# Performance work log

Measured on AMD Instinct MI355X. Metric: run time of the kernel, lower is better.

## Reference

```python
import jax, jax.numpy as jnp
import numpy as np
from jax import lax

EPS = 1e-5
DN = ('NCDHW', 'OIDHW', 'NCDHW')


def _instance_norm(x, w, b):
    # normalize over spatial dims per (batch, channel); biased variance like torch
    mu = jnp.mean(x, axis=(2, 3, 4), keepdims=True)
    var = jnp.mean((x - mu) ** 2, axis=(2, 3, 4), keepdims=True)
    xn = (x - mu) * lax.rsqrt(var + EPS)
    return xn * w[None, :, None, None, None] + b[None, :, None, None, None]


def _conv1x1(x, w, b):
    # w: [Cout, Cin]
    y = jnp.einsum('bcdhw,oc->bodhw', x, w)
    return y + b[None, :, None, None, None]


def _dwconv3(x, w, b):
    # depthwise 3x3x3, padding 1; w: [C, 1, 3, 3, 3]
    y = lax.conv_general_dilated(x, w, (1, 1, 1), 'SAME',
                                 dimension_numbers=DN,
                                 feature_group_count=w.shape[0])
    return y + b[None, :, None, None, None]


def setup_inputs() -> dict:
    key = jax.random.key(0)
    ks = jax.random.split(key, 8)
    C, half = 64, 32
    B, D, H, W = 1, 96, 96, 96
    s1 = 1.0 / np.sqrt(C)          # fan_in of 1x1 conv
    s3 = 1.0 / np.sqrt(27.0)       # fan_in of depthwise 3x3x3
    return {
        'x': jax.random.normal(ks[0], (B, C, D, H, W), jnp.float32),
        'norm_w': jnp.ones((C,), jnp.float32),
        'norm_b': jnp.zeros((C,), jnp.float32),
        'in_proj_w': jax.random.normal(ks[1], (C, C), jnp.float32) * s1,
        'in_proj_b': jnp.zeros((C,), jnp.float32),
        'conv_ssm_w': jax.random.normal(ks[2], (half, 1, 3, 3, 3), jnp.float32) * s3,
        'conv_ssm_b': jnp.zeros((half,), jnp.float32),
        'mamba_w': jax.random.normal(ks[3], (half, 1, 3, 3, 3), jnp.float32) * s3,
        'mamba_b': jnp.zeros((half,), jnp.float32),
        'conv_sym_w': jax.random.normal(ks[4], (half, 1, 3, 3, 3), jnp.float32) * s3,
        'conv_sym_b': jnp.zeros((half,), jnp.float32),
        'out_proj_w': jax.random.normal(ks[5], (C, C), jnp.float32) * s1,
        'out_proj_b': jnp.zeros((C,), jnp.float32),
    }


def reference(x, norm_w, norm_b, in_proj_w, in_proj_b,
              conv_ssm_w, conv_ssm_b, mamba_w, mamba_b,
              conv_sym_w, conv_sym_b, out_proj_w, out_proj_b):
    residual = x
    xp = _conv1x1(_instance_norm(x, norm_w, norm_b), in_proj_w, in_proj_b)
    half = xp.shape[1] // 2
    x1, x2 = xp[:, :half], xp[:, half:]
    # SSM branch (TriDirectionalMamba fallback = depthwise conv3)
    x1 = _dwconv3(jax.nn.silu(_dwconv3(x1, conv_ssm_w, conv_ssm_b)), mamba_w, mamba_b)
    # symmetric conv branch
    x2 = jax.nn.silu(_dwconv3(x2, conv_sym_w, conv_sym_b))
    y = _conv1x1(jnp.concatenate([x1, x2], axis=1), out_proj_w, out_proj_b)
    return y + residual
```

## Files before the change

### kernel.cpp

```cpp
#include <hip/hip_runtime.h>

typedef unsigned short u16;
typedef unsigned int u32;
typedef short bf16x8 __attribute__((ext_vector_type(8)));
typedef float f32x16 __attribute__((ext_vector_type(16)));
typedef u16 u16x8 __attribute__((ext_vector_type(8)));

#define DIM 96
#define PLANE (DIM*DIM)
#define S 884736
#define C 64
#define HALF 32
#define PARTS 16
#define EPS 1e-5f
#define DSPLIT 4
#define DCHUNK (DIM/DSPLIT)

#define RPAD 104
#define LROWS 18
#define LBUF (8 + LROWS*RPAD)

#define MFMA32(a,b,c) __builtin_amdgcn_mfma_f32_32x32x16_bf16(a,b,c,0,0,0)

__device__ __forceinline__ u16 f2bf(float f) {
  u32 u = __builtin_bit_cast(u32, f);
  return (u16)((u + 0x7FFFu + ((u >> 16) & 1u)) >> 16);
}
__device__ __forceinline__ float bf2f(u16 h) {
  return __builtin_bit_cast(float, (u32)h << 16);
}
__device__ __forceinline__ u32 cvt_pk_bf16(float lo, float hi) {
  u32 r;
  asm("v_cvt_pk_bf16_f32 %0, %1, %2" : "=v"(r) : "v"(lo), "v"(hi));
  return r;
}
__device__ __forceinline__ float silu(float v) { return v / (1.f + __expf(-v)); }
__device__ __forceinline__ u16x8 zero8() {
  u16x8 z;
  #pragma unroll
  for (int i = 0; i < 8; ++i) z[i] = 0;
  return z;
}

__global__ __launch_bounds__(256) void k1_stats(const float* __restrict__ x,
                                                u16* __restrict__ xb,
                                                float* __restrict__ psum,
                                                float* __restrict__ psq) {
  const int bid = blockIdx.x;
  const int ch = bid / PARTS, part = bid % PARTS;
  const int chunk = S / PARTS;
  const size_t base = (size_t)ch * S + (size_t)part * chunk;
  const float4* p = (const float4*)(x + base);
  ushort4* xb4 = (ushort4*)(xb + base);
  const int n4 = chunk / 4;
  float s = 0.f, q = 0.f;
  for (int i = threadIdx.x; i < n4; i += 256) {
    float4 v = p[i];
    s += (v.x + v.y) + (v.z + v.w);
    q += (v.x * v.x + v.y * v.y) + (v.z * v.z + v.w * v.w);
    union { u32 u[2]; ushort4 v4; } o;
    o.u[0] = cvt_pk_bf16(v.x, v.y);
    o.u[1] = cvt_pk_bf16(v.z, v.w);
    xb4[i] = o.v4;
  }
  #pragma unroll
  for (int off = 32; off > 0; off >>= 1) {
    s += __shfl_down(s, off);
    q += __shfl_down(q, off);
  }
  __shared__ float ls[4], lq[4];
  const int wid = threadIdx.x >> 6, lane = threadIdx.x & 63;
  if (lane == 0) { ls[wid] = s; lq[wid] = q; }
  __syncthreads();
  if (threadIdx.x == 0) {
    psum[bid] = (ls[0] + ls[1]) + (ls[2] + ls[3]);
    psq[bid]  = (lq[0] + lq[1]) + (lq[2] + lq[3]);
  }
}

__global__ __launch_bounds__(64) void k1b_prep(const float* __restrict__ psum,
    const float* __restrict__ psq,
    const float* __restrict__ norm_w, const float* __restrict__ norm_b,
    const float* __restrict__ in_w, const float* __restrict__ in_b,
    const float* __restrict__ out_w,
    u16* __restrict__ Wp, float* __restrict__ biasp, u16* __restrict__ Wo) {
  __shared__ float a_s[C], b2_s[C];
  const int t = threadIdx.x;
  float s = 0.f, q = 0.f;
  for (int i = 0; i < PARTS; ++i) { s += psum[t * PARTS + i]; q += psq[t * PARTS + i]; }
  const float inv = 1.f / (float)S;
  const float mu = s * inv;
  const float var = q * inv - mu * mu;
  const float rsig = rsqrtf(var + EPS);
  const float a = norm_w[t] * rsig;
  const float b2 = norm_b[t] - mu * a;
  a_s[t] = a; b2_s[t] = b2;
  __syncthreads();
  float bp = in_b[t];
  for (int c = 0; c < C; ++c) {
    const float w = in_w[t * C + c];
    Wp[t * C + c] = f2bf(w * a_s[c]);
    bp += b2_s[c] * w;
    Wo[t * C + c] = f2bf(out_w[t * C + c]);
  }
  biasp[t] = bp;
}

__global__ __launch_bounds__(256) void k2_mfma(const u16* __restrict__ xb,
    const u16* __restrict__ Wp, const float* __restrict__ biasp,
    u16* __restrict__ xp) {
  const int lane = threadIdx.x & 63, wid = threadIdx.x >> 6;
  const int n = lane & 31, hf = lane >> 5;
  const int v0 = blockIdx.x * 256 + wid * 64;
  bf16x8 A[2][4];
  #pragma unroll
  for (int t = 0; t < 2; ++t)
    #pragma unroll
    for (int s = 0; s < 4; ++s)
      A[t][s] = *(const bf16x8*)(Wp + (t * 32 + n) * C + s * 16 + hf * 8);

  f32x16 accE[2], accO[2];
  #pragma unroll
  for (int t = 0; t < 2; ++t)
    #pragma unroll
    for (int r = 0; r < 16; ++r) {
      const float b = biasp[t * 32 + (r & 3) + 8 * (r >> 2) + 4 * hf];
      accE[t][r] = b; accO[t][r] = b;
    }

  #pragma unroll
  for (int s = 0; s < 4; ++s) {
    union { u16 u[8]; bf16x8 v; } BE, BO;
    #pragma unroll
    for (int j = 0; j < 8; ++j) {
      const u32 xv = *(const u32*)(xb + (size_t)(s * 16 + hf * 8 + j) * S + v0 + 2 * n);
      BE.u[j] = (u16)(xv & 0xFFFFu); BO.u[j] = (u16)(xv >> 16);
    }
    #pragma unroll
    for (int t = 0; t < 2; ++t) {
      accE[t] = MFMA32(A[t][s], BE.v, accE[t]);
      accO[t] = MFMA32(A[t][s], BO.v, accO[t]);
    }
  }
  #pragma unroll
  for (int t = 0; t < 2; ++t)
    #pragma unroll
    for (int r = 0; r < 16; ++r) {
      const int o = t * 32 + (r & 3) + 8 * (r >> 2) + 4 * hf;
      *(u32*)(xp + (size_t)o * S + v0 + 2 * n) = cvt_pk_bf16(accE[t][r], accO[t][r]);
    }
}

__device__ __forceinline__ void fma3(float* __restrict__ a,
    const float* __restrict__ r, float t0, float t1, float t2) {
  #pragma unroll
  for (int i = 0; i < 8; ++i) a[i] = fmaf(t0, r[i], a[i]);
  #pragma unroll
  for (int i = 0; i < 8; ++i) a[i] = fmaf(t1, r[i + 1], a[i]);
  #pragma unroll
  for (int i = 0; i < 8; ++i) a[i] = fmaf(t2, r[i + 2], a[i]);
}

template<bool SILU>
__global__ __launch_bounds__(192) void dwconv(const u16* __restrict__ srcA,
    const float* __restrict__ kwA, const float* __restrict__ bA,
    u16* __restrict__ dstA,
    const float* __restrict__ kwB, const float* __restrict__ bB,
    u16* __restrict__ dstB) {
  __shared__ u16 lds[2][LBUF];
  const int c = blockIdx.z;
  const u16* src = srcA + (size_t)c * S;
  u16* dst; const float* kwp; float bias;
  if (c < HALF) { dst = dstA + (size_t)c * S;          kwp = kwA + c * 27;          bias = bA[c]; }
  else          { dst = dstB + (size_t)(c - HALF) * S; kwp = kwB + (c - HALF) * 27; bias = bB[c - HALF]; }
  float kw[27];
  #pragma unroll
  for (int i = 0; i < 27; ++i) kw[i] = kwp[i];

  const int tx = threadIdx.x, ty = threadIdx.y;
  const int tid = ty * 12 + tx;
  const int w8 = tx * 8;
  const int h0 = blockIdx.x * 16;
  const int d0 = blockIdx.y * DCHUNK;

  if (tid < 38) {
    const int b = tid / 19, k = tid % 19;
    *(u16x8*)&lds[b][RPAD * k] = zero8();
  }

  const int s_row0 = tid / 12, s_cc0 = tid % 12;
  const int s_row1 = (192 + tid) / 12, s_cc1 = (192 + tid) % 12;
  const bool has2 = tid < 24;
  const int s_h0 = h0 - 1 + s_row0;
  const int s_h1 = h0 - 1 + s_row1;
  const bool h0ok = (unsigned)s_h0 < DIM;
  const bool h1ok = has2 && ((unsigned)s_h1 < DIM);
  u16x8 vs0, vs1;

  #define STAGE_LOAD(DD) { \
    vs0 = zero8(); vs1 = zero8(); \
    if (((unsigned)(DD) < DIM) && h0ok) \
      vs0 = *(const u16x8*)(src + (size_t)(DD) * PLANE + s_h0 * DIM + s_cc0 * 8); \
    if (((unsigned)(DD) < DIM) && h1ok) \
      vs1 = *(const u16x8*)(src + (size_t)(DD) * PLANE + s_h1 * DIM + s_cc1 * 8); }

  #define STAGE_WRITE(WB) { \
    *(u16x8*)&lds[WB][8 + s_row0 * RPAD + s_cc0 * 8] = vs0; \
    if (has2) *(u16x8*)&lds[WB][8 + s_row1 * RPAD + s_cc1 * 8] = vs1; }

  float r0[10], r1[10], r2[10];
  float A[8], B[8], o8[8];

  #define LOADROW(R, ROWI, RB) { \
    const u16* _lb = &lds[RB][8 + (ROWI) * RPAD + w8]; \
    const u16x8 _m = *(const u16x8*)_lb; \
    const u16 _lo = _lb[-1], _hi = _lb[8]; \
    R[0] = bf2f(_lo); \
    _Pragma("unroll") \
    for (int i = 0; i < 8; ++i) R[1 + i] = bf2f(_m[i]); \
    R[9] = bf2f(_hi); }

  #define LOADROWS(RB) { LOADROW(r0, ty, RB); LOADROW(r1, ty + 1, RB); LOADROW(r2, ty + 2, RB); }

  #define CBLK(ACC, K0) { \
    fma3(ACC, r0, kw[(K0) + 0], kw[(K0) + 1], kw[(K0) + 2]); \
    fma3(ACC, r1, kw[(K0) + 3], kw[(K0) + 4], kw[(K0) + 5]); \
    fma3(ACC, r2, kw[(K0) + 6], kw[(K0) + 7], kw[(K0) + 8]); }

  STAGE_LOAD(d0 - 1);
  STAGE_WRITE(0);
  __syncthreads();

  LOADROWS(0);
  STAGE_LOAD(d0);
  #pragma unroll
  for (int i = 0; i < 8; ++i) B[i] = bias;
  CBLK(B, 0);
  STAGE_WRITE(1);
  __syncthreads();

  LOADROWS(1);
  STAGE_LOAD(d0 + 1);
  #pragma unroll
  for (int i = 0; i < 8; ++i) { A[i] = B[i]; B[i] = bias; }
  CBLK(A, 9);
  CBLK(B, 0);
  STAGE_WRITE(0);
  __syncthreads();

  u16* db = dst + (size_t)d0 * PLANE + (size_t)(h0 + ty) * DIM + w8;

  #define ROUND_BODY(D, RB, WB, DO_STG) { \
    LOADROWS(RB); \
    if (DO_STG) STAGE_LOAD((D) + 2); \
    _Pragma("unroll") \
    for (int i = 0; i < 8; ++i) o8[i] = A[i]; \
    CBLK(o8, 18); \
    _Pragma("unroll") \
    for (int i = 0; i < 8; ++i) A[i] = B[i]; \
    CBLK(A, 9); \
    _Pragma("unroll") \
    for (int i = 0; i < 8; ++i) B[i] = bias; \
    CBLK(B, 0); \
    if (SILU) { \
      _Pragma("unroll") \
      for (int i = 0; i < 8; ++i) o8[i] = silu(o8[i]); \
    } \
    union { u32 u[4]; u16x8 v; } _o; \
    _Pragma("unroll") \
    for (int i = 0; i < 4; ++i) _o.u[i] = cvt_pk_bf16(o8[2 * i], o8[2 * i + 1]); \
    *(u16x8*)db = _o.v; \
    db += PLANE; \
    if (DO_STG) STAGE_WRITE(WB); \
    __syncthreads(); }

  #pragma unroll 1
  for (int d = d0; d < d0 + DCHUNK; d += 2) {
    ROUND_BODY(d, 0, 1, true);
    ROUND_BODY(d + 1, 1, 0, (d + 2) < d0 + DCHUNK);
  }
  #undef ROUND_BODY
  #undef CBLK
  #undef LOADROWS
  #undef LOADROW
  #undef STAGE_WRITE
  #undef STAGE_LOAD
}

__global__ __launch_bounds__(256) void k4b_mfma(const u16* __restrict__ z_lo,
    const u16* __restrict__ z_hi, const u16* __restrict__ xb,
    const u16* __restrict__ Wo, const float* __restrict__ ob,
    float* __restrict__ out) {
  const int lane = threadIdx.x & 63, wid = threadIdx.x >> 6;
  const int n = lane & 31, hf = lane >> 5;
  const int v0 = blockIdx.x * 256 + wid * 64;
  bf16x8 A[2][4];
  #pragma unroll
  for (int t = 0; t < 2; ++t)
    #pragma unroll
    for (int s = 0; s < 4; ++s)
      A[t][s] = *(const bf16x8*)(Wo + (t * 32 + n) * C + s * 16 + hf * 8);

  f32x16 accE[2], accO[2];
  #pragma unroll
  for (int t = 0; t < 2; ++t)
    #pragma unroll
    for (int r = 0; r < 16; ++r) {
      const float b = ob[t * 32 + (r & 3) + 8 * (r >> 2) + 4 * hf];
      accE[t][r] = b; accO[t][r] = b;
    }

  #pragma unroll
  for (int s = 0; s < 4; ++s) {
    const u16* zbase = (s < 2) ? z_lo + (size_t)(s * 16) * S
                               : z_hi + (size_t)((s - 2) * 16) * S;
    union { u16 u[8]; bf16x8 v; } BE, BO;
    #pragma unroll
    for (int j = 0; j < 8; ++j) {
      const u32 zv = *(const u32*)(zbase + (size_t)(hf * 8 + j) * S + v0 + 2 * n);
      BE.u[j] = (u16)(zv & 0xFFFFu); BO.u[j] = (u16)(zv >> 16);
    }
    #pragma unroll
    for (int t = 0; t < 2; ++t) {
      accE[t] = MFMA32(A[t][s], BE.v, accE[t]);
      accO[t] = MFMA32(A[t][s], BO.v, accO[t]);
    }
  }
  #pragma unroll
  for (int t = 0; t < 2; ++t)
    #pragma unroll
    for (int r = 0; r < 16; ++r) {
      const int o = t * 32 + (r & 3) + 8 * (r >> 2) + 4 * hf;
      const u32 xr = *(const u32*)(xb + (size_t)o * S + v0 + 2 * n);
      float2 ov;
      ov.x = accE[t][r] + bf2f((u16)(xr & 0xFFFFu));
      ov.y = accO[t][r] + bf2f((u16)(xr >> 16));
      *(float2*)(out + (size_t)o * S + v0 + 2 * n) = ov;
    }
}

extern "C" void kernel_launch(void* const* d_in, const int* in_sizes, int n_in,
                              void* d_out, int out_size, void* d_ws, size_t ws_size,
                              hipStream_t stream) {
  const float* x      = (const float*)d_in[0];
  const float* norm_w = (const float*)d_in[1];
  const float* norm_b = (const float*)d_in[2];
  const float* in_w   = (const float*)d_in[3];
  const float* in_b   = (const float*)d_in[4];
  const float* ssm_w  = (const float*)d_in[5];
  const float* ssm_b  = (const float*)d_in[6];
  const float* mam_w  = (const float*)d_in[7];
  const float* mam_b  = (const float*)d_in[8];
  const float* sym_w  = (const float*)d_in[9];
  const float* sym_b  = (const float*)d_in[10];
  const float* out_w  = (const float*)d_in[11];
  const float* out_b  = (const float*)d_in[12];
  float* out = (float*)d_out;

  u16* xb   = (u16*)d_ws;
  u16* xp   = xb + (size_t)C * S;
  u16* t1   = xp + (size_t)C * S;
  u16* z_hi = t1 + (size_t)HALF * S;
  u16* z_lo = xp;
  float* psum  = (float*)(z_hi + (size_t)HALF * S);
  float* psq   = psum + C * PARTS;
  u16* Wp      = (u16*)(psq + C * PARTS);
  u16* Wo      = Wp + C * C;
  float* biasp = (float*)(Wo + C * C);

  k1_stats<<<C * PARTS, 256, 0, stream>>>(x, xb, psum, psq);
  k1b_prep<<<1, 64, 0, stream>>>(psum, psq, norm_w, norm_b, in_w, in_b, out_w,
                                 Wp, biasp, Wo);
  k2_mfma<<<S / 256, 256, 0, stream>>>(xb, Wp, biasp, xp);
  dwconv<true><<<dim3(DIM / 16, DSPLIT, C), dim3(12, 16, 1), 0, stream>>>(
      xp, ssm_w, ssm_b, t1, sym_w, sym_b, z_hi);
  dwconv<false><<<dim3(DIM / 16, DSPLIT, HALF), dim3(12, 16, 1), 0, stream>>>(
      t1, mam_w, mam_b, z_lo, mam_w, mam_b, z_lo);
  k4b_mfma<<<S / 256, 256, 0, stream>>>(z_lo, z_hi, xb, Wo, out_b, out);
}
```

Before: 354.1 us.

## Widen MFMA pointwise kernels to four voxels per lane and store dwconv LDS as fp32

The 1x1-conv MFMA kernels now have each lane load four adjacent voxels (8-byte loads, 16-byte fp32 output stores) and keep four accumulator tiles, halving the grid. The goal is wider global memory transactions and more MFMA work per weight load. Separately, the depthwise conv stages its LDS tile as fp32 instead of bf16, converting once at write time rather than on every row read, at the cost of doubling the LDS footprint and adding register pressure.

```diff
diff --git a/kernel.cpp b/kernel.cpp
--- a/kernel.cpp
+++ b/kernel.cpp
@@ -16,9 +16,9 @@
 #define DSPLIT 4
 #define DCHUNK (DIM/DSPLIT)
 
-#define RPAD 104
+#define RPADF 108
 #define LROWS 18
-#define LBUF (8 + LROWS*RPAD)
+#define LBUFF (LROWS*RPADF)
 
 #define MFMA32(a,b,c) __builtin_amdgcn_mfma_f32_32x32x16_bf16(a,b,c,0,0,0)
 
@@ -111,7 +111,7 @@
     u16* __restrict__ xp) {
   const int lane = threadIdx.x & 63, wid = threadIdx.x >> 6;
   const int n = lane & 31, hf = lane >> 5;
-  const int v0 = blockIdx.x * 256 + wid * 64;
+  const int v0 = blockIdx.x * 512 + wid * 128;
   bf16x8 A[2][4];
   #pragma unroll
   for (int t = 0; t < 2; ++t)
@@ -119,35 +119,39 @@
     for (int s = 0; s < 4; ++s)
       A[t][s] = *(const bf16x8*)(Wp + (t * 32 + n) * C + s * 16 + hf * 8);
 
-  f32x16 accE[2], accO[2];
+  f32x16 acc[2][4];
   #pragma unroll
   for (int t = 0; t < 2; ++t)
     #pragma unroll
     for (int r = 0; r < 16; ++r) {
       const float b = biasp[t * 32 + (r & 3) + 8 * (r >> 2) + 4 * hf];
-      accE[t][r] = b; accO[t][r] = b;
+      #pragma unroll
+      for (int q = 0; q < 4; ++q) acc[t][q][r] = b;
     }
 
   #pragma unroll
   for (int s = 0; s < 4; ++s) {
-    union { u16 u[8]; bf16x8 v; } BE, BO;
+    union { u16 u[8]; bf16x8 v; } Bq[4];
     #pragma unroll
     for (int j = 0; j < 8; ++j) {
-      const u32 xv = *(const u32*)(xb + (size_t)(s * 16 + hf * 8 + j) * S + v0 + 2 * n);
-      BE.u[j] = (u16)(xv & 0xFFFFu); BO.u[j] = (u16)(xv >> 16);
-    }
-    #pragma unroll
-    for (int t = 0; t < 2; ++t) {
-      accE[t] = MFMA32(A[t][s], BE.v, accE[t]);
-      accO[t] = MFMA32(A[t][s], BO.v, accO[t]);
-    }
+      const ushort4 zv = *(const ushort4*)(xb + (size_t)(s * 16 + hf * 8 + j) * S + v0 + 4 * n);
+      Bq[0].u[j] = zv.x; Bq[1].u[j] = zv.y; Bq[2].u[j] = zv.z; Bq[3].u[j] = zv.w;
+    }
+    #pragma unroll
+    for (int t = 0; t < 2; ++t)
+      #pragma unroll
+      for (int q = 0; q < 4; ++q)
+        acc[t][q] = MFMA32(A[t][s], Bq[q].v, acc[t][q]);
   }
   #pragma unroll
   for (int t = 0; t < 2; ++t)
     #pragma unroll
     for (int r = 0; r < 16; ++r) {
       const int o = t * 32 + (r & 3) + 8 * (r >> 2) + 4 * hf;
-      *(u32*)(xp + (size_t)o * S + v0 + 2 * n) = cvt_pk_bf16(accE[t][r], accO[t][r]);
+      union { u32 u[2]; ushort4 v4; } pr;
+      pr.u[0] = cvt_pk_bf16(acc[t][0][r], acc[t][1][r]);
+      pr.u[1] = cvt_pk_bf16(acc[t][2][r], acc[t][3][r]);
+      *(ushort4*)(xp + (size_t)o * S + v0 + 4 * n) = pr.v4;
     }
 }
 
@@ -167,7 +171,7 @@
     u16* __restrict__ dstA,
     const float* __restrict__ kwB, const float* __restrict__ bB,
     u16* __restrict__ dstB) {
-  __shared__ u16 lds[2][LBUF];
+  __shared__ float lds[2][LBUFF];
   const int c = blockIdx.z;
   const u16* src = srcA + (size_t)c * S;
   u16* dst; const float* kwp; float bias;
@@ -183,9 +187,12 @@
   const int h0 = blockIdx.x * 16;
   const int d0 = blockIdx.y * DCHUNK;
 
-  if (tid < 38) {
-    const int b = tid / 19, k = tid % 19;
-    *(u16x8*)&lds[b][RPAD * k] = zero8();
+  if (tid < 36) {
+    const int b = tid / 18, r = tid % 18;
+    float4 z4 = make_float4(0.f, 0.f, 0.f, 0.f);
+    *(float4*)&lds[b][r * RPADF + 0] = z4;
+    *(float4*)&lds[b][r * RPADF + 4] = z4;
+    *(float4*)&lds[b][r * RPADF + 104] = z4;
   }
 
   const int s_row0 = tid / 12, s_cc0 = tid % 12;
@@ -205,20 +212,28 @@
       vs1 = *(const u16x8*)(src + (size_t)(DD) * PLANE + s_h1 * DIM + s_cc1 * 8); }
 
   #define STAGE_WRITE(WB) { \
-    *(u16x8*)&lds[WB][8 + s_row0 * RPAD + s_cc0 * 8] = vs0; \
-    if (has2) *(u16x8*)&lds[WB][8 + s_row1 * RPAD + s_cc1 * 8] = vs1; }
+    float4 f0, f1; \
+    f0.x = bf2f(vs0[0]); f0.y = bf2f(vs0[1]); f0.z = bf2f(vs0[2]); f0.w = bf2f(vs0[3]); \
+    f1.x = bf2f(vs0[4]); f1.y = bf2f(vs0[5]); f1.z = bf2f(vs0[6]); f1.w = bf2f(vs0[7]); \
+    *(float4*)&lds[WB][8 + s_row0 * RPADF + s_cc0 * 8] = f0; \
+    *(float4*)&lds[WB][8 + s_row0 * RPADF + s_cc0 * 8 + 4] = f1; \
+    if (has2) { \
+      f0.x = bf2f(vs1[0]); f0.y = bf2f(vs1[1]); f0.z = bf2f(vs1[2]); f0.w = bf2f(vs1[3]); \
+      f1.x = bf2f(vs1[4]); f1.y = bf2f(vs1[5]); f1.z = bf2f(vs1[6]); f1.w = bf2f(vs1[7]); \
+      *(float4*)&lds[WB][8 + s_row1 * RPADF + s_cc1 * 8] = f0; \
+      *(float4*)&lds[WB][8 + s_row1 * RPADF + s_cc1 * 8 + 4] = f1; } }
 
   float r0[10], r1[10], r2[10];
   float A[8], B[8], o8[8];
 
   #define LOADROW(R, ROWI, RB) { \
-    const u16* _lb = &lds[RB][8 + (ROWI) * RPAD + w8]; \
-    const u16x8 _m = *(const u16x8*)_lb; \
-    const u16 _lo = _lb[-1], _hi = _lb[8]; \
-    R[0] = bf2f(_lo); \
-    _Pragma("unroll") \
-    for (int i = 0; i < 8; ++i) R[1 + i] = bf2f(_m[i]); \
-    R[9] = bf2f(_hi); }
+    const float* _lb = &lds[RB][8 + (ROWI) * RPADF + w8]; \
+    const float4 _a = *(const float4*)_lb; \
+    const float4 _b = *(const float4*)(_lb + 4); \
+    R[0] = _lb[-1]; \
+    R[1] = _a.x; R[2] = _a.y; R[3] = _a.z; R[4] = _a.w; \
+    R[5] = _b.x; R[6] = _b.y; R[7] = _b.z; R[8] = _b.w; \
+    R[9] = _lb[8]; }
 
   #define LOADROWS(RB) { LOADROW(r0, ty, RB); LOADROW(r1, ty + 1, RB); LOADROW(r2, ty + 2, RB); }
 
@@ -293,7 +308,7 @@
     float* __restrict__ out) {
   const int lane = threadIdx.x & 63, wid = threadIdx.x >> 6;
   const int n = lane & 31, hf = lane >> 5;
-  const int v0 = blockIdx.x * 256 + wid * 64;
+  const int v0 = blockIdx.x * 512 + wid * 128;
   bf16x8 A[2][4];
   #pragma unroll
   for (int t = 0; t < 2; ++t)
@@ -301,41 +316,44 @@
     for (int s = 0; s < 4; ++s)
       A[t][s] = *(const bf16x8*)(Wo + (t * 32 + n) * C + s * 16 + hf * 8);
 
-  f32x16 accE[2], accO[2];
+  f32x16 acc[2][4];
   #pragma unroll
   for (int t = 0; t < 2; ++t)
     #pragma unroll
     for (int r = 0; r < 16; ++r) {
       const float b = ob[t * 32 + (r & 3) + 8 * (r >> 2) + 4 * hf];
-      accE[t][r] = b; accO[t][r] = b;
+      #pragma unroll
+      for (int q = 0; q < 4; ++q) acc[t][q][r] = b;
     }
 
   #pragma unroll
   for (int s = 0; s < 4; ++s) {
     const u16* zbase = (s < 2) ? z_lo + (size_t)(s * 16) * S
                                : z_hi + (size_t)((s - 2) * 16) * S;
-    union { u16 u[8]; bf16x8 v; } BE, BO;
+    union { u16 u[8]; bf16x8 v; } Bq[4];
     #pragma unroll
     for (int j = 0; j < 8; ++j) {
-      const u32 zv = *(const u32*)(zbase + (size_t)(hf * 8 + j) * S + v0 + 2 * n);
-      BE.u[j] = (u16)(zv & 0xFFFFu); BO.u[j] = (u16)(zv >> 16);
-    }
-    #pragma unroll
-    for (int t = 0; t < 2; ++t) {
-      accE[t] = MFMA32(A[t][s], BE.v, accE[t]);
-      accO[t] = MFMA32(A[t][s], BO.v, accO[t]);
-    }
+      const ushort4 zv = *(const ushort4*)(zbase + (size_t)(hf * 8 + j) * S + v0 + 4 * n);
+      Bq[0].u[j] = zv.x; Bq[1].u[j] = zv.y; Bq[2].u[j] = zv.z; Bq[3].u[j] = zv.w;
+    }
+    #pragma unroll
+    for (int t = 0; t < 2; ++t)
+      #pragma unroll
+      for (int q = 0; q < 4; ++q)
+        acc[t][q] = MFMA32(A[t][s], Bq[q].v, acc[t][q]);
   }
   #pragma unroll
   for (int t = 0; t < 2; ++t)
     #pragma unroll
     for (int r = 0; r < 16; ++r) {
       const int o = t * 32 + (r & 3) + 8 * (r >> 2) + 4 * hf;
-      const u32 xr = *(const u32*)(xb + (size_t)o * S + v0 + 2 * n);
-      float2 ov;
-      ov.x = accE[t][r] + bf2f((u16)(xr & 0xFFFFu));
-      ov.y = accO[t][r] + bf2f((u16)(xr >> 16));
-      *(float2*)(out + (size_t)o * S + v0 + 2 * n) = ov;
+      const ushort4 xr = *(const ushort4*)(xb + (size_t)o * S + v0 + 4 * n);
+      float4 ov;
+      ov.x = acc[t][0][r] + bf2f(xr.x);
+      ov.y = acc[t][1][r] + bf2f(xr.y);
+      ov.z = acc[t][2][r] + bf2f(xr.z);
+      ov.w = acc[t][3][r] + bf2f(xr.w);
+      *(float4*)(out + (size_t)o * S + v0 + 4 * n) = ov;
     }
 }
 
@@ -371,10 +389,10 @@
   k1_stats<<<C * PARTS, 256, 0, stream>>>(x, xb, psum, psq);
   k1b_prep<<<1, 64, 0, stream>>>(psum, psq, norm_w, norm_b, in_w, in_b, out_w,
                                  Wp, biasp, Wo);
-  k2_mfma<<<S / 256, 256, 0, stream>>>(xb, Wp, biasp, xp);
+  k2_mfma<<<S / 512, 256, 0, stream>>>(xb, Wp, biasp, xp);
   dwconv<true><<<dim3(DIM / 16, DSPLIT, C), dim3(12, 16, 1), 0, stream>>>(
       xp, ssm_w, ssm_b, t1, sym_w, sym_b, z_hi);
   dwconv<false><<<dim3(DIM / 16, DSPLIT, HALF), dim3(12, 16, 1), 0, stream>>>(
       t1, mam_w, mam_b, z_lo, mam_w, mam_b, z_lo);
-  k4b_mfma<<<S / 256, 256, 0, stream>>>(z_lo, z_hi, xb, Wo, out_b, out);
-}
+  k4b_mfma<<<S / 512, 256, 0, stream>>>(z_lo, z_hi, xb, Wo, out_b, out);
+}
```

Result: slower. 363.3 us (+2.6%).
